# Kernel optimization log

Hardware: AMD Instinct MI355X
Metric: run time of the kernel (lower is better)

Reference implementation:

```python
import jax, jax.numpy as jnp
import numpy as np
from jax import lax

B, DIM, H, W = 4, 192, 128, 128
NUM_HEADS = 4
EPS = 1e-12


def _conv1x1(x, w):
    # x: [b,c,h,w], w: [o,i,1,1]
    return lax.conv_general_dilated(x, w, (1, 1), 'VALID',
                                    dimension_numbers=('NCHW', 'OIHW', 'NCHW'))


def _dwconv3x3(x, w):
    # depthwise: w: [c,1,3,3], groups = c
    return lax.conv_general_dilated(x, w, (1, 1), ((1, 1), (1, 1)),
                                    dimension_numbers=('NCHW', 'OIHW', 'NCHW'),
                                    feature_group_count=w.shape[0])


def _l2norm(t):
    # normalize along last (spatial) axis, torch F.normalize semantics
    n = jnp.sqrt(jnp.sum(t * t, axis=-1, keepdims=True))
    return t / jnp.maximum(n, EPS)


def _heads(t, b, h, w):
    # [b, head*c, h, w] -> [b, head, c, h*w]
    return t.reshape(b, NUM_HEADS, t.shape[1] // NUM_HEADS, h * w)


def setup_inputs() -> dict:
    key = jax.random.key(0)
    ks = jax.random.split(key, 9)
    s = 0.02
    return {
        'x': jax.random.normal(ks[0], (B, DIM, H, W), jnp.float32),
        'ctx': jax.random.normal(ks[1], (B, DIM, H, W), jnp.float32),
        'x_qkv_w': jax.random.normal(ks[2], (DIM * 3, DIM, 1, 1), jnp.float32) * s,
        'x_dw_w': jax.random.normal(ks[3], (DIM * 3, 1, 3, 3), jnp.float32) * s,
        'x_po_w': jax.random.normal(ks[4], (DIM, DIM, 1, 1), jnp.float32) * s,
        'ctx_qkv_w': jax.random.normal(ks[5], (DIM * 3, DIM, 1, 1), jnp.float32) * s,
        'ctx_dw_w': jax.random.normal(ks[6], (DIM * 3, 1, 3, 3), jnp.float32) * s,
        'ctx_po_w': jax.random.normal(ks[7], (DIM, DIM, 1, 1), jnp.float32) * s,
        'temperature': jnp.ones((NUM_HEADS, 1, 1), jnp.float32),
    }


def reference(x, ctx, x_qkv_w, x_dw_w, x_po_w, ctx_qkv_w, ctx_dw_w, ctx_po_w, temperature):
    b, c, h, w = x.shape
    x_qkv = _dwconv3x3(_conv1x1(x, x_qkv_w), x_dw_w)
    x_q, x_k, x_v = jnp.split(x_qkv, 3, axis=1)
    ctx_qkv = _dwconv3x3(_conv1x1(ctx, ctx_qkv_w), ctx_dw_w)
    ctx_q, ctx_k, ctx_v = jnp.split(ctx_qkv, 3, axis=1)

    x_q, x_k, x_v = (_heads(t, b, h, w) for t in (x_q, x_k, x_v))
    ctx_q, ctx_k, ctx_v = (_heads(t, b, h, w) for t in (ctx_q, ctx_k, ctx_v))

    temp = temperature[None]  # [1, head, 1, 1]

    # ctx branch: x_q attends over ctx
    q1 = _l2norm(x_q)
    k1 = _l2norm(ctx_k)
    attn1 = jax.nn.softmax(jnp.einsum('bhcn,bhdn->bhcd', q1, k1) * temp, axis=-1)
    ctx_out = jnp.einsum('bhcd,bhdn->bhcn', attn1, ctx_v).reshape(b, c, h, w)
    ctx_out = _conv1x1(ctx_out, ctx_po_w)

    # x branch: ctx_q attends over x
    q2 = _l2norm(ctx_q)
    k2 = _l2norm(x_k)
    attn2 = jax.nn.softmax(jnp.einsum('bhcn,bhdn->bhcd', q2, k2) * temp, axis=-1)
    x_out = jnp.einsum('bhcd,bhdn->bhcn', attn2, x_v).reshape(b, c, h, w)
    x_out = _conv1x1(x_out, x_po_w)

    return (x_out, ctx_out)
```

## Files before the change

### kernel.cpp

```cpp
#include <hip/hip_runtime.h>
#include <hip/hip_bf16.h>

#define N_PIX 16384
#define W_ 128

typedef __attribute__((ext_vector_type(8))) unsigned short ushort8_t;
typedef __attribute__((ext_vector_type(4))) unsigned short ushort4_t;
typedef __attribute__((ext_vector_type(8))) __bf16 bf16x8;
typedef __attribute__((ext_vector_type(4))) float f32x4;

__device__ inline float bf2f(unsigned short u) {
    return __uint_as_float(((unsigned)u) << 16);
}
__device__ inline unsigned short f2bf(float f) {
    __hip_bfloat16 h = __float2bfloat16(f);
    return *(unsigned short*)&h;
}

__global__ __launch_bounds__(256) void k_pack_w(
    const float* __restrict__ wa, const float* __restrict__ wb,
    unsigned short* __restrict__ oa, unsigned short* __restrict__ ob)
{
    const int blk = blockIdx.x;
    const float* w = (blk < 108) ? wa : wb;
    unsigned short* o = (blk < 108) ? oa : ob;
    const int i = ((blk % 108) * 256 + threadIdx.x) * 4;
    float4 v = *(const float4*)(w + i);
    ushort4_t s;
    s[0] = f2bf(v.x); s[1] = f2bf(v.y); s[2] = f2bf(v.z); s[3] = f2bf(v.w);
    *(ushort4_t*)(o + i) = s;
}

__global__ __launch_bounds__(512, 2) void k_conv_mfma(
    const float* __restrict__ x, const float* __restrict__ ctx,
    const unsigned short* __restrict__ wx, const unsigned short* __restrict__ wc,
    unsigned short* __restrict__ ox, unsigned short* __restrict__ octx)
{
    const int p0 = blockIdx.x * 128;
    const int bb = blockIdx.y;
    const int b  = bb & 3;
    const bool isx = bb < 4;
    const float* inb = (isx ? x : ctx) + (long)b * 192 * N_PIX;
    const unsigned short* wbf = isx ? wx : wc;
    unsigned short* ob = (isx ? ox : octx) + (long)b * 576 * N_PIX;

    __shared__ unsigned short Xl[128 * 200];

    const int tid  = threadIdx.x;
    const int lane = tid & 63;
    const int wid  = tid >> 6;
    const int wo   = wid >> 1;
    const int wp   = wid & 1;
    const int l15  = lane & 15;
    const int lq   = lane >> 4;

    {
        const int p = tid & 127, kh = tid >> 7;
        #pragma unroll
        for (int seg = 0; seg < 6; seg++) {
            ushort8_t pk;
            #pragma unroll
            for (int j = 0; j < 8; j++)
                pk[j] = f2bf(inb[(long)(kh * 48 + seg * 8 + j) * N_PIX + p0 + p]);
            *(ushort8_t*)&Xl[p * 200 + kh * 48 + seg * 8] = pk;
        }
    }
    __syncthreads();

    #pragma unroll 1
    for (int oc = 0; oc < 3; oc++) {
        const unsigned short* wrow = wbf + (long)(oc * 192 + wo * 48) * 192;

        bf16x8 afA[3], afB[3];
        #pragma unroll
        for (int mt = 0; mt < 3; mt++)
            afA[mt] = *(const bf16x8*)(wrow + (mt * 16 + l15) * 192 + lq * 8);

        f32x4 acc[3][4];
        const f32x4 zero = {0.f, 0.f, 0.f, 0.f};
        #pragma unroll
        for (int i = 0; i < 3; i++)
            #pragma unroll
            for (int j = 0; j < 4; j++) acc[i][j] = zero;

        #pragma unroll 1
        for (int kc2 = 0; kc2 < 3; kc2++) {
            const int kcA = kc2 * 2, kcB = kcA + 1;
            #pragma unroll
            for (int mt = 0; mt < 3; mt++)
                afB[mt] = *(const bf16x8*)(wrow + (mt * 16 + l15) * 192 + kcB * 32 + lq * 8);
            {
                bf16x8 bfv[4];
                #pragma unroll
                for (int nt = 0; nt < 4; nt++)
                    bfv[nt] = *(const bf16x8*)&Xl[(wp * 64 + nt * 16 + l15) * 200 + kcA * 32 + lq * 8];
                #pragma unroll
                for (int mt = 0; mt < 3; mt++)
                    #pragma unroll
                    for (int nt = 0; nt < 4; nt++)
                        acc[mt][nt] = __builtin_amdgcn_mfma_f32_16x16x32_bf16(
                            afA[mt], bfv[nt], acc[mt][nt], 0, 0, 0);
            }
            if (kc2 < 2) {
                #pragma unroll
                for (int mt = 0; mt < 3; mt++)
                    afA[mt] = *(const bf16x8*)(wrow + (mt * 16 + l15) * 192 + (kcA + 2) * 32 + lq * 8);
            }
            {
                bf16x8 bfv[4];
                #pragma unroll
                for (int nt = 0; nt < 4; nt++)
                    bfv[nt] = *(const bf16x8*)&Xl[(wp * 64 + nt * 16 + l15) * 200 + kcB * 32 + lq * 8];
                #pragma unroll
                for (int mt = 0; mt < 3; mt++)
                    #pragma unroll
                    for (int nt = 0; nt < 4; nt++)
                        acc[mt][nt] = __builtin_amdgcn_mfma_f32_16x16x32_bf16(
                            afB[mt], bfv[nt], acc[mt][nt], 0, 0, 0);
            }
        }

        #pragma unroll
        for (int mt = 0; mt < 3; mt++) {
            #pragma unroll
            for (int r = 0; r < 4; r++) {
                int o = oc * 192 + wo * 48 + mt * 16 + lq * 4 + r;
                long base = (long)o * N_PIX + p0 + wp * 64 + l15;
                #pragma unroll
                for (int nt = 0; nt < 4; nt++)
                    ob[base + nt * 16] = f2bf(acc[mt][nt][r]);
            }
        }
    }
}

__global__ __launch_bounds__(256) void k_dwconv(
    const unsigned short* __restrict__ tx, const unsigned short* __restrict__ tc,
    const float* __restrict__ wxd, const float* __restrict__ wcd,
    unsigned short* __restrict__ qx, unsigned short* __restrict__ qc)
{
    const int mz = blockIdx.y;
    const int br = (mz >= 2304) ? 1 : 0;
    const int m  = mz - br * 2304;
    const int ch = m % 576;
    const int y0 = blockIdx.x * 16;
    const unsigned short* ip = (br ? tc : tx) + (long)m * N_PIX;
    const float* wp = (br ? wcd : wxd) + ch * 9;
    unsigned short* op = (br ? qc : qx) + (long)m * N_PIX;

    __shared__ unsigned short Ll[18][136];

    const int tid = threadIdx.x;
    #pragma unroll
    for (int idx = tid; idx < 288; idx += 256) {
        int lr = idx >> 4, lc = (idx & 15) * 8;
        int gy = y0 - 1 + lr;
        ushort8_t v;
        #pragma unroll
        for (int j = 0; j < 8; j++) v[j] = 0;
        if ((unsigned)gy <= 127u)
            v = *(const ushort8_t*)(ip + gy * W_ + lc);
        *(ushort8_t*)&Ll[lr][lc] = v;
    }
    float wv[9];
    #pragma unroll
    for (int i = 0; i < 9; i++) wv[i] = wp[i];
    __syncthreads();

    const int r  = tid >> 4;
    const int xg = (tid & 15) * 8;

    float o[8];
    #pragma unroll
    for (int j = 0; j < 8; j++) o[j] = 0.f;

    #pragma unroll
    for (int dy = 0; dy < 3; dy++) {
        const unsigned short* lrow = &Ll[r + dy][0];
        float c[10];
        c[0] = (xg == 0) ? 0.f : bf2f(lrow[xg - 1]);
        ushort8_t mid = *(const ushort8_t*)&lrow[xg];
        #pragma unroll
        for (int j = 0; j < 8; j++) c[1 + j] = bf2f(mid[j]);
        c[9] = (xg == 120) ? 0.f : bf2f(lrow[xg + 8]);
        const float w0 = wv[dy * 3], w1 = wv[dy * 3 + 1], w2 = wv[dy * 3 + 2];
        #pragma unroll
        for (int j = 0; j < 8; j++)
            o[j] = fmaf(w0, c[j], fmaf(w1, c[j + 1], fmaf(w2, c[j + 2], o[j])));
    }
    ushort8_t res;
    #pragma unroll
    for (int j = 0; j < 8; j++) res[j] = f2bf(o[j]);
    *(ushort8_t*)(op + (y0 + r) * W_ + xg) = res;
}

__global__ __launch_bounds__(256) void k_gram_mfma(
    const unsigned short* __restrict__ qkv_x,
    const unsigned short* __restrict__ qkv_c,
    float* __restrict__ S, float* __restrict__ qn, float* __restrict__ kn)
{
    const int attn = blockIdx.z;
    const int bh   = blockIdx.y;
    const int b = bh >> 2, h = bh & 3;
    const unsigned short* qb =
        (attn == 0 ? qkv_x : qkv_c) + ((long)b * 576 + h * 48) * N_PIX;
    const unsigned short* kb =
        (attn == 0 ? qkv_c : qkv_x) + ((long)b * 576 + 192 + h * 48) * N_PIX;

    __shared__ float Sl[48 * 49];
    __shared__ float qnl[48], knl[48];

    const int tid = threadIdx.x;
    for (int i = tid; i < 48 * 49; i += 256) Sl[i] = 0.f;
    if (tid < 48) { qnl[tid] = 0.f; knl[tid] = 0.f; }
    __syncthreads();

    const int lane = tid & 63, wid = tid >> 6;
    const int l15 = lane & 15, lq = lane >> 4;
    const long nbase = (long)blockIdx.x * 1024 + wid * 256;

    f32x4 acc[3][3], aq[3], ak[3];
    const f32x4 zero = {0.f, 0.f, 0.f, 0.f};
    #pragma unroll
    for (int i = 0; i < 3; i++) {
        aq[i] = zero; ak[i] = zero;
        #pragma unroll
        for (int j = 0; j < 3; j++) acc[i][j] = zero;
    }

    for (int ks = 0; ks < 8; ks++) {
        const long ns = nbase + ks * 32;
        bf16x8 af[3], bfv[3];
        #pragma unroll
        for (int mt = 0; mt < 3; mt++)
            af[mt] = *(const bf16x8*)(qb + (long)(mt * 16 + l15) * N_PIX + ns + lq * 8);
        #pragma unroll
        for (int nt = 0; nt < 3; nt++)
            bfv[nt] = *(const bf16x8*)(kb + (long)(nt * 16 + l15) * N_PIX + ns + lq * 8);
        #pragma unroll
        for (int mt = 0; mt < 3; mt++)
            #pragma unroll
            for (int nt = 0; nt < 3; nt++)
                acc[mt][nt] = __builtin_amdgcn_mfma_f32_16x16x32_bf16(
                    af[mt], bfv[nt], acc[mt][nt], 0, 0, 0);
        #pragma unroll
        for (int mt = 0; mt < 3; mt++)
            aq[mt] = __builtin_amdgcn_mfma_f32_16x16x32_bf16(af[mt], af[mt], aq[mt], 0, 0, 0);
        #pragma unroll
        for (int nt = 0; nt < 3; nt++)
            ak[nt] = __builtin_amdgcn_mfma_f32_16x16x32_bf16(bfv[nt], bfv[nt], ak[nt], 0, 0, 0);
    }

    #pragma unroll
    for (int mt = 0; mt < 3; mt++)
        #pragma unroll
        for (int nt = 0; nt < 3; nt++)
            #pragma unroll
            for (int r = 0; r < 4; r++)
                atomicAdd(&Sl[(mt * 16 + lq * 4 + r) * 49 + nt * 16 + l15],
                          acc[mt][nt][r]);
    #pragma unroll
    for (int mt = 0; mt < 3; mt++)
        #pragma unroll
        for (int r = 0; r < 4; r++)
            if (l15 == lq * 4 + r) {
                atomicAdd(&qnl[mt * 16 + l15], aq[mt][r]);
                atomicAdd(&knl[mt * 16 + l15], ak[mt][r]);
            }
    __syncthreads();

    float* Sg = S + (long)(attn * 16 + bh) * 2304;
    float* qg = qn + (long)(attn * 16 + bh) * 48;
    float* kg = kn + (long)(attn * 16 + bh) * 48;
    for (int i = tid; i < 2304; i += 256) {
        int row = i / 48, col = i - row * 48;
        atomicAdd(&Sg[i], Sl[row * 49 + col]);
    }
    if (tid < 48) atomicAdd(&qg[tid], qnl[tid]);
    else if (tid < 96) atomicAdd(&kg[tid - 48], knl[tid - 48]);
}

__global__ __launch_bounds__(192) void k_softmax(
    const float* __restrict__ S, const float* __restrict__ qn,
    const float* __restrict__ kn, const float* __restrict__ temp,
    float* __restrict__ P)
{
    const int attn = blockIdx.x, b = blockIdx.y;
    const int r = threadIdx.x;
    const int h = r / 48, c = r % 48;
    const int bh = b * 4 + h;
    const float t = temp[h];
    const float* Srow = S + ((long)(attn * 16 + bh) * 48 + c) * 48;
    const float* knp  = kn + (long)(attn * 16 + bh) * 48;
    const float qc = fmaxf(sqrtf(qn[(long)(attn * 16 + bh) * 48 + c]), 1e-12f);
    float lg[48];
    float mx = -1e30f;
    #pragma unroll
    for (int d = 0; d < 48; d++) {
        float kd = fmaxf(sqrtf(knp[d]), 1e-12f);
        lg[d] = Srow[d] / (qc * kd) * t;
        mx = fmaxf(mx, lg[d]);
    }
    float sum = 0.f;
    #pragma unroll
    for (int d = 0; d < 48; d++) { lg[d] = __expf(lg[d] - mx); sum += lg[d]; }
    const float inv = 1.f / sum;
    float* Pp = P + (((long)(attn * 4 + b) * 4 + h) * 48 + c) * 48;
    #pragma unroll
    for (int d = 0; d < 48; d++) Pp[d] = lg[d] * inv;
}

__global__ __launch_bounds__(192) void k_w2(
    const float* __restrict__ P, const float* __restrict__ x_po,
    const float* __restrict__ ctx_po, unsigned short* __restrict__ W2)
{
    const int h = blockIdx.x, b = blockIdx.y, attn = blockIdx.z;
    const float* po = (attn == 0) ? ctx_po : x_po;
    __shared__ float Pl[48][48];
    const float* Pp = P + ((long)(attn * 4 + b) * 4 + h) * 2304;
    for (int it = 0; it < 12; it++) {
        int idx = it * 192 + threadIdx.x;
        Pl[idx / 48][idx % 48] = Pp[idx];
    }
    __syncthreads();
    const int o = threadIdx.x;
    float acc[48];
    #pragma unroll
    for (int d = 0; d < 48; d++) acc[d] = 0.f;
    for (int c = 0; c < 48; c++) {
        float pv = po[(long)o * 192 + h * 48 + c];
        #pragma unroll
        for (int d = 0; d < 48; d++)
            acc[d] = fmaf(pv, Pl[c][d], acc[d]);
    }
    unsigned short* wp = W2 + ((long)(attn * 4 + b) * 192 + o) * 192 + h * 48;
    #pragma unroll
    for (int d = 0; d < 48; d++) wp[d] = f2bf(acc[d]);
}

__global__ __launch_bounds__(512, 2) void k_gemm_v(
    const unsigned short* __restrict__ qkv_x,
    const unsigned short* __restrict__ qkv_c,
    const unsigned short* __restrict__ W2bf,
    float* __restrict__ out)
{
    const int p0 = blockIdx.x * 128;
    const int z  = blockIdx.y;
    const int br = z >> 2, b = z & 3;
    const unsigned short* v =
        (br == 0 ? qkv_x : qkv_c) + (long)b * 576 * N_PIX + 384L * N_PIX;
    const unsigned short* wb =
        W2bf + ((long)((br == 0 ? 1 : 0) * 4 + b)) * 36864;
    float* ob = out + (long)br * 12582912 + (long)b * 192 * N_PIX;

    __shared__ unsigned short Xl[128 * 200];

    const int tid  = threadIdx.x;
    const int lane = tid & 63;
    const int wid  = tid >> 6;
    const int wo   = wid >> 1;
    const int wp   = wid & 1;
    const int l15  = lane & 15;
    const int lq   = lane >> 4;

    {
        const int p = tid & 127, kh = tid >> 7;
        #pragma unroll
        for (int seg = 0; seg < 6; seg++) {
            ushort8_t pk;
            #pragma unroll
            for (int j = 0; j < 8; j++)
                pk[j] = v[(long)(kh * 48 + seg * 8 + j) * N_PIX + p0 + p];
            *(ushort8_t*)&Xl[p * 200 + kh * 48 + seg * 8] = pk;
        }
    }
    __syncthreads();

    const unsigned short* wrow = wb + (long)(wo * 48) * 192;

    bf16x8 afA[3], afB[3];
    #pragma unroll
    for (int mt = 0; mt < 3; mt++)
        afA[mt] = *(const bf16x8*)(wrow + (mt * 16 + l15) * 192 + lq * 8);

    f32x4 acc[3][4];
    const f32x4 zero = {0.f, 0.f, 0.f, 0.f};
    #pragma unroll
    for (int i = 0; i < 3; i++)
        #pragma unroll
        for (int j = 0; j < 4; j++) acc[i][j] = zero;

    #pragma unroll 1
    for (int kc2 = 0; kc2 < 3; kc2++) {
        const int kcA = kc2 * 2, kcB = kcA + 1;
        #pragma unroll
        for (int mt = 0; mt < 3; mt++)
            afB[mt] = *(const bf16x8*)(wrow + (mt * 16 + l15) * 192 + kcB * 32 + lq * 8);
        {
            bf16x8 bfv[4];
            #pragma unroll
            for (int nt = 0; nt < 4; nt++)
                bfv[nt] = *(const bf16x8*)&Xl[(wp * 64 + nt * 16 + l15) * 200 + kcA * 32 + lq * 8];
            #pragma unroll
            for (int mt = 0; mt < 3; mt++)
                #pragma unroll
                for (int nt = 0; nt < 4; nt++)
                    acc[mt][nt] = __builtin_amdgcn_mfma_f32_16x16x32_bf16(
                        afA[mt], bfv[nt], acc[mt][nt], 0, 0, 0);
        }
        if (kc2 < 2) {
            #pragma unroll
            for (int mt = 0; mt < 3; mt++)
                afA[mt] = *(const bf16x8*)(wrow + (mt * 16 + l15) * 192 + (kcA + 2) * 32 + lq * 8);
        }
        {
            bf16x8 bfv[4];
            #pragma unroll
            for (int nt = 0; nt < 4; nt++)
                bfv[nt] = *(const bf16x8*)&Xl[(wp * 64 + nt * 16 + l15) * 200 + kcB * 32 + lq * 8];
            #pragma unroll
            for (int mt = 0; mt < 3; mt++)
                #pragma unroll
                for (int nt = 0; nt < 4; nt++)
                    acc[mt][nt] = __builtin_amdgcn_mfma_f32_16x16x32_bf16(
                        afB[mt], bfv[nt], acc[mt][nt], 0, 0, 0);
        }
    }

    #pragma unroll
    for (int mt = 0; mt < 3; mt++) {
        #pragma unroll
        for (int r = 0; r < 4; r++) {
            int o = wo * 48 + mt * 16 + lq * 4 + r;
            long base = (long)o * N_PIX + p0 + wp * 64 + l15;
            #pragma unroll
            for (int nt = 0; nt < 4; nt++)
                ob[base + nt * 16] = acc[mt][nt][r];
        }
    }
}

extern "C" void kernel_launch(void* const* d_in, const int* in_sizes, int n_in,
                              void* d_out, int out_size, void* d_ws, size_t ws_size,
                              hipStream_t stream) {
    (void)in_sizes; (void)n_in; (void)out_size;
    const float* x       = (const float*)d_in[0];
    const float* ctx     = (const float*)d_in[1];
    const float* x_qkv_w = (const float*)d_in[2];
    const float* x_dw_w  = (const float*)d_in[3];
    const float* x_po_w  = (const float*)d_in[4];
    const float* c_qkv_w = (const float*)d_in[5];
    const float* c_dw_w  = (const float*)d_in[6];
    const float* c_po_w  = (const float*)d_in[7];
    const float* temp    = (const float*)d_in[8];
    float* out = (float*)d_out;

    const long QKV = 37748736L;
    unsigned short* qkv_x16 = (unsigned short*)d_ws;
    unsigned short* qkv_c16 = qkv_x16 + QKV;
    float* S  = (float*)(qkv_c16 + QKV);
    float* qn = S + 73728;
    float* kn = qn + 1536;
    float* P  = kn + 1536;
    unsigned short* W2bf = (unsigned short*)(P + 73728);

    unsigned short* tmp_x = (unsigned short*)d_out;
    unsigned short* wx16  = (unsigned short*)d_out + QKV;
    unsigned short* wc16  = wx16 + 110592;

    k_pack_w<<<dim3(216), 256, 0, stream>>>(x_qkv_w, c_qkv_w, wx16, wc16);

    const size_t ws_needed = (size_t)QKV * 2 * 3;
    if (ws_size >= ws_needed) {
        unsigned short* tmp_c = (unsigned short*)S;
        k_conv_mfma<<<dim3(128, 8), 512, 0, stream>>>(
            x, ctx, wx16, wc16, tmp_x, tmp_c);
        k_dwconv<<<dim3(8, 4608), 256, 0, stream>>>(
            tmp_x, tmp_c, x_dw_w, c_dw_w, qkv_x16, qkv_c16);
    } else {
        k_conv_mfma<<<dim3(128, 4), 512, 0, stream>>>(
            x, x, wx16, wx16, tmp_x, tmp_x);
        k_dwconv<<<dim3(8, 2304), 256, 0, stream>>>(
            tmp_x, tmp_x, x_dw_w, x_dw_w, qkv_x16, qkv_x16);
        k_conv_mfma<<<dim3(128, 4), 512, 0, stream>>>(
            ctx, ctx, wc16, wc16, tmp_x, tmp_x);
        k_dwconv<<<dim3(8, 2304), 256, 0, stream>>>(
            tmp_x, tmp_x, c_dw_w, c_dw_w, qkv_c16, qkv_c16);
    }

    hipMemsetAsync(S, 0, (73728 + 1536 + 1536) * sizeof(float), stream);

    k_gram_mfma<<<dim3(16, 16, 2), 256, 0, stream>>>(qkv_x16, qkv_c16, S, qn, kn);
    k_softmax<<<dim3(2, 4), dim3(192), 0, stream>>>(S, qn, kn, temp, P);
    k_w2<<<dim3(4, 4, 2), dim3(192), 0, stream>>>(P, x_po_w, c_po_w, W2bf);

    k_gemm_v<<<dim3(128, 8), 512, 0, stream>>>(qkv_x16, qkv_c16, W2bf, out);
}
```

Measured before the change: 412.2 us.

## Halve pixel tiles in conv and V-GEMM kernels; fuse softmax with W2 build

The 1x1-conv and final V-GEMM kernels now run 256-thread blocks over 64-pixel tiles instead of 512-thread blocks over 128 pixels. This doubles the grid size and allows more resident blocks per CU, while the MFMA inner loop loads one B fragment at a time to lower register pressure. The softmax and P·W_po kernels are merged into one kernel that keeps P in shared memory, which removes a launch and the global round trip for P. The trade-off is that each fused block runs four heads serially on only 8 blocks, and each weight fragment is reused across fewer pixels.

```diff
diff --git a/kernel.cpp b/kernel.cpp
--- a/kernel.cpp
+++ b/kernel.cpp
@@ -31,12 +31,12 @@
     *(ushort4_t*)(o + i) = s;
 }
 
-__global__ __launch_bounds__(512, 2) void k_conv_mfma(
+__global__ __launch_bounds__(256, 4) void k_conv_mfma(
     const float* __restrict__ x, const float* __restrict__ ctx,
     const unsigned short* __restrict__ wx, const unsigned short* __restrict__ wc,
     unsigned short* __restrict__ ox, unsigned short* __restrict__ octx)
 {
-    const int p0 = blockIdx.x * 128;
+    const int p0 = blockIdx.x * 64;
     const int bb = blockIdx.y;
     const int b  = bb & 3;
     const bool isx = bb < 4;
@@ -44,18 +44,16 @@
     const unsigned short* wbf = isx ? wx : wc;
     unsigned short* ob = (isx ? ox : octx) + (long)b * 576 * N_PIX;
 
-    __shared__ unsigned short Xl[128 * 200];
+    __shared__ unsigned short Xl[64 * 200];
 
     const int tid  = threadIdx.x;
     const int lane = tid & 63;
-    const int wid  = tid >> 6;
-    const int wo   = wid >> 1;
-    const int wp   = wid & 1;
+    const int wo   = tid >> 6;
     const int l15  = lane & 15;
     const int lq   = lane >> 4;
 
     {
-        const int p = tid & 127, kh = tid >> 7;
+        const int p = tid & 63, kh = tid >> 6;
         #pragma unroll
         for (int seg = 0; seg < 6; seg++) {
             ushort8_t pk;
@@ -89,34 +87,26 @@
             #pragma unroll
             for (int mt = 0; mt < 3; mt++)
                 afB[mt] = *(const bf16x8*)(wrow + (mt * 16 + l15) * 192 + kcB * 32 + lq * 8);
-            {
-                bf16x8 bfv[4];
-                #pragma unroll
-                for (int nt = 0; nt < 4; nt++)
-                    bfv[nt] = *(const bf16x8*)&Xl[(wp * 64 + nt * 16 + l15) * 200 + kcA * 32 + lq * 8];
+            #pragma unroll
+            for (int nt = 0; nt < 4; nt++) {
+                bf16x8 bfv = *(const bf16x8*)&Xl[(nt * 16 + l15) * 200 + kcA * 32 + lq * 8];
                 #pragma unroll
                 for (int mt = 0; mt < 3; mt++)
-                    #pragma unroll
-                    for (int nt = 0; nt < 4; nt++)
-                        acc[mt][nt] = __builtin_amdgcn_mfma_f32_16x16x32_bf16(
-                            afA[mt], bfv[nt], acc[mt][nt], 0, 0, 0);
+                    acc[mt][nt] = __builtin_amdgcn_mfma_f32_16x16x32_bf16(
+                        afA[mt], bfv, acc[mt][nt], 0, 0, 0);
             }
             if (kc2 < 2) {
                 #pragma unroll
                 for (int mt = 0; mt < 3; mt++)
                     afA[mt] = *(const bf16x8*)(wrow + (mt * 16 + l15) * 192 + (kcA + 2) * 32 + lq * 8);
             }
-            {
-                bf16x8 bfv[4];
-                #pragma unroll
-                for (int nt = 0; nt < 4; nt++)
-                    bfv[nt] = *(const bf16x8*)&Xl[(wp * 64 + nt * 16 + l15) * 200 + kcB * 32 + lq * 8];
+            #pragma unroll
+            for (int nt = 0; nt < 4; nt++) {
+                bf16x8 bfv = *(const bf16x8*)&Xl[(nt * 16 + l15) * 200 + kcB * 32 + lq * 8];
                 #pragma unroll
                 for (int mt = 0; mt < 3; mt++)
-                    #pragma unroll
-                    for (int nt = 0; nt < 4; nt++)
-                        acc[mt][nt] = __builtin_amdgcn_mfma_f32_16x16x32_bf16(
-                            afB[mt], bfv[nt], acc[mt][nt], 0, 0, 0);
+                    acc[mt][nt] = __builtin_amdgcn_mfma_f32_16x16x32_bf16(
+                        afB[mt], bfv, acc[mt][nt], 0, 0, 0);
             }
         }
 
@@ -125,7 +115,7 @@
             #pragma unroll
             for (int r = 0; r < 4; r++) {
                 int o = oc * 192 + wo * 48 + mt * 16 + lq * 4 + r;
-                long base = (long)o * N_PIX + p0 + wp * 64 + l15;
+                long base = (long)o * N_PIX + p0 + l15;
                 #pragma unroll
                 for (int nt = 0; nt < 4; nt++)
                     ob[base + nt * 16] = f2bf(acc[mt][nt][r]);
@@ -280,71 +270,68 @@
     else if (tid < 96) atomicAdd(&kg[tid - 48], knl[tid - 48]);
 }
 
-__global__ __launch_bounds__(192) void k_softmax(
+__global__ __launch_bounds__(192) void k_sm_w2(
     const float* __restrict__ S, const float* __restrict__ qn,
     const float* __restrict__ kn, const float* __restrict__ temp,
-    float* __restrict__ P)
+    const float* __restrict__ x_po, const float* __restrict__ ctx_po,
+    unsigned short* __restrict__ W2)
 {
     const int attn = blockIdx.x, b = blockIdx.y;
-    const int r = threadIdx.x;
-    const int h = r / 48, c = r % 48;
-    const int bh = b * 4 + h;
-    const float t = temp[h];
-    const float* Srow = S + ((long)(attn * 16 + bh) * 48 + c) * 48;
-    const float* knp  = kn + (long)(attn * 16 + bh) * 48;
-    const float qc = fmaxf(sqrtf(qn[(long)(attn * 16 + bh) * 48 + c]), 1e-12f);
-    float lg[48];
-    float mx = -1e30f;
-    #pragma unroll
-    for (int d = 0; d < 48; d++) {
-        float kd = fmaxf(sqrtf(knp[d]), 1e-12f);
-        lg[d] = Srow[d] / (qc * kd) * t;
-        mx = fmaxf(mx, lg[d]);
-    }
-    float sum = 0.f;
-    #pragma unroll
-    for (int d = 0; d < 48; d++) { lg[d] = __expf(lg[d] - mx); sum += lg[d]; }
-    const float inv = 1.f / sum;
-    float* Pp = P + (((long)(attn * 4 + b) * 4 + h) * 48 + c) * 48;
-    #pragma unroll
-    for (int d = 0; d < 48; d++) Pp[d] = lg[d] * inv;
-}
-
-__global__ __launch_bounds__(192) void k_w2(
-    const float* __restrict__ P, const float* __restrict__ x_po,
-    const float* __restrict__ ctx_po, unsigned short* __restrict__ W2)
-{
-    const int h = blockIdx.x, b = blockIdx.y, attn = blockIdx.z;
-    const float* po = (attn == 0) ? ctx_po : x_po;
-    __shared__ float Pl[48][48];
-    const float* Pp = P + ((long)(attn * 4 + b) * 4 + h) * 2304;
-    for (int it = 0; it < 12; it++) {
-        int idx = it * 192 + threadIdx.x;
-        Pl[idx / 48][idx % 48] = Pp[idx];
-    }
-    __syncthreads();
-    const int o = threadIdx.x;
-    float acc[48];
-    #pragma unroll
-    for (int d = 0; d < 48; d++) acc[d] = 0.f;
-    for (int c = 0; c < 48; c++) {
-        float pv = po[(long)o * 192 + h * 48 + c];
-        #pragma unroll
-        for (int d = 0; d < 48; d++)
-            acc[d] = fmaf(pv, Pl[c][d], acc[d]);
-    }
-    unsigned short* wp = W2 + ((long)(attn * 4 + b) * 192 + o) * 192 + h * 48;
-    #pragma unroll
-    for (int d = 0; d < 48; d++) wp[d] = f2bf(acc[d]);
-}
-
-__global__ __launch_bounds__(512, 2) void k_gemm_v(
+    __shared__ float Pl[4][48][48];
+
+    {
+        const int r = threadIdx.x;
+        const int h = r / 48, c = r % 48;
+        const int bh = b * 4 + h;
+        const float t = temp[h];
+        const float* Srow = S + ((long)(attn * 16 + bh) * 48 + c) * 48;
+        const float* knp  = kn + (long)(attn * 16 + bh) * 48;
+        const float qc = fmaxf(sqrtf(qn[(long)(attn * 16 + bh) * 48 + c]), 1e-12f);
+        float lg[48];
+        float mx = -1e30f;
+        #pragma unroll
+        for (int d = 0; d < 48; d++) {
+            float kd = fmaxf(sqrtf(knp[d]), 1e-12f);
+            lg[d] = Srow[d] / (qc * kd) * t;
+            mx = fmaxf(mx, lg[d]);
+        }
+        float sum = 0.f;
+        #pragma unroll
+        for (int d = 0; d < 48; d++) { lg[d] = __expf(lg[d] - mx); sum += lg[d]; }
+        const float inv = 1.f / sum;
+        #pragma unroll
+        for (int d = 0; d < 48; d++) Pl[h][c][d] = lg[d] * inv;
+    }
+    __syncthreads();
+
+    {
+        const float* po = (attn == 0) ? ctx_po : x_po;
+        const int o = threadIdx.x;
+        unsigned short* wp = W2 + ((long)(attn * 4 + b) * 192 + o) * 192;
+        #pragma unroll 1
+        for (int h = 0; h < 4; h++) {
+            float acc[48];
+            #pragma unroll
+            for (int d = 0; d < 48; d++) acc[d] = 0.f;
+            for (int c = 0; c < 48; c++) {
+                float pv = po[(long)o * 192 + h * 48 + c];
+                #pragma unroll
+                for (int d = 0; d < 48; d++)
+                    acc[d] = fmaf(pv, Pl[h][c][d], acc[d]);
+            }
+            #pragma unroll
+            for (int d = 0; d < 48; d++) wp[h * 48 + d] = f2bf(acc[d]);
+        }
+    }
+}
+
+__global__ __launch_bounds__(256, 4) void k_gemm_v(
     const unsigned short* __restrict__ qkv_x,
     const unsigned short* __restrict__ qkv_c,
     const unsigned short* __restrict__ W2bf,
     float* __restrict__ out)
 {
-    const int p0 = blockIdx.x * 128;
+    const int p0 = blockIdx.x * 64;
     const int z  = blockIdx.y;
     const int br = z >> 2, b = z & 3;
     const unsigned short* v =
@@ -353,18 +340,16 @@
         W2bf + ((long)((br == 0 ? 1 : 0) * 4 + b)) * 36864;
     float* ob = out + (long)br * 12582912 + (long)b * 192 * N_PIX;
 
-    __shared__ unsigned short Xl[128 * 200];
+    __shared__ unsigned short Xl[64 * 200];
 
     const int tid  = threadIdx.x;
     const int lane = tid & 63;
-    const int wid  = tid >> 6;
-    const int wo   = wid >> 1;
-    const int wp   = wid & 1;
+    const int wo   = tid >> 6;
     const int l15  = lane & 15;
     const int lq   = lane >> 4;
 
     {
-        const int p = tid & 127, kh = tid >> 7;
+        const int p = tid & 63, kh = tid >> 6;
         #pragma unroll
         for (int seg = 0; seg < 6; seg++) {
             ushort8_t pk;
@@ -396,34 +381,26 @@
         #pragma unroll
         for (int mt = 0; mt < 3; mt++)
             afB[mt] = *(const bf16x8*)(wrow + (mt * 16 + l15) * 192 + kcB * 32 + lq * 8);
-        {
-            bf16x8 bfv[4];
-            #pragma unroll
-            for (int nt = 0; nt < 4; nt++)
-                bfv[nt] = *(const bf16x8*)&Xl[(wp * 64 + nt * 16 + l15) * 200 + kcA * 32 + lq * 8];
+        #pragma unroll
+        for (int nt = 0; nt < 4; nt++) {
+            bf16x8 bfv = *(const bf16x8*)&Xl[(nt * 16 + l15) * 200 + kcA * 32 + lq * 8];
             #pragma unroll
             for (int mt = 0; mt < 3; mt++)
-                #pragma unroll
-                for (int nt = 0; nt < 4; nt++)
-                    acc[mt][nt] = __builtin_amdgcn_mfma_f32_16x16x32_bf16(
-                        afA[mt], bfv[nt], acc[mt][nt], 0, 0, 0);
+                acc[mt][nt] = __builtin_amdgcn_mfma_f32_16x16x32_bf16(
+                    afA[mt], bfv, acc[mt][nt], 0, 0, 0);
         }
         if (kc2 < 2) {
             #pragma unroll
             for (int mt = 0; mt < 3; mt++)
                 afA[mt] = *(const bf16x8*)(wrow + (mt * 16 + l15) * 192 + (kcA + 2) * 32 + lq * 8);
         }
-        {
-            bf16x8 bfv[4];
-            #pragma unroll
-            for (int nt = 0; nt < 4; nt++)
-                bfv[nt] = *(const bf16x8*)&Xl[(wp * 64 + nt * 16 + l15) * 200 + kcB * 32 + lq * 8];
+        #pragma unroll
+        for (int nt = 0; nt < 4; nt++) {
+            bf16x8 bfv = *(const bf16x8*)&Xl[(nt * 16 + l15) * 200 + kcB * 32 + lq * 8];
             #pragma unroll
             for (int mt = 0; mt < 3; mt++)
-                #pragma unroll
-                for (int nt = 0; nt < 4; nt++)
-                    acc[mt][nt] = __builtin_amdgcn_mfma_f32_16x16x32_bf16(
-                        afB[mt], bfv[nt], acc[mt][nt], 0, 0, 0);
+                acc[mt][nt] = __builtin_amdgcn_mfma_f32_16x16x32_bf16(
+                    afB[mt], bfv, acc[mt][nt], 0, 0, 0);
         }
     }
 
@@ -432,7 +409,7 @@
         #pragma unroll
         for (int r = 0; r < 4; r++) {
             int o = wo * 48 + mt * 16 + lq * 4 + r;
-            long base = (long)o * N_PIX + p0 + wp * 64 + l15;
+            long base = (long)o * N_PIX + p0 + l15;
             #pragma unroll
             for (int nt = 0; nt < 4; nt++)
                 ob[base + nt * 16] = acc[mt][nt][r];
@@ -461,8 +438,7 @@
     float* S  = (float*)(qkv_c16 + QKV);
     float* qn = S + 73728;
     float* kn = qn + 1536;
-    float* P  = kn + 1536;
-    unsigned short* W2bf = (unsigned short*)(P + 73728);
+    unsigned short* W2bf = (unsigned short*)(kn + 1536);
 
     unsigned short* tmp_x = (unsigned short*)d_out;
     unsigned short* wx16  = (unsigned short*)d_out + QKV;
@@ -473,16 +449,16 @@
     const size_t ws_needed = (size_t)QKV * 2 * 3;
     if (ws_size >= ws_needed) {
         unsigned short* tmp_c = (unsigned short*)S;
-        k_conv_mfma<<<dim3(128, 8), 512, 0, stream>>>(
+        k_conv_mfma<<<dim3(256, 8), 256, 0, stream>>>(
             x, ctx, wx16, wc16, tmp_x, tmp_c);
         k_dwconv<<<dim3(8, 4608), 256, 0, stream>>>(
             tmp_x, tmp_c, x_dw_w, c_dw_w, qkv_x16, qkv_c16);
     } else {
-        k_conv_mfma<<<dim3(128, 4), 512, 0, stream>>>(
+        k_conv_mfma<<<dim3(256, 4), 256, 0, stream>>>(
             x, x, wx16, wx16, tmp_x, tmp_x);
         k_dwconv<<<dim3(8, 2304), 256, 0, stream>>>(
             tmp_x, tmp_x, x_dw_w, x_dw_w, qkv_x16, qkv_x16);
-        k_conv_mfma<<<dim3(128, 4), 512, 0, stream>>>(
+        k_conv_mfma<<<dim3(256, 4), 256, 0, stream>>>(
             ctx, ctx, wc16, wc16, tmp_x, tmp_x);
         k_dwconv<<<dim3(8, 2304), 256, 0, stream>>>(
             tmp_x, tmp_x, c_dw_w, c_dw_w, qkv_c16, qkv_c16);
@@ -491,8 +467,8 @@
     hipMemsetAsync(S, 0, (73728 + 1536 + 1536) * sizeof(float), stream);
 
     k_gram_mfma<<<dim3(16, 16, 2), 256, 0, stream>>>(qkv_x16, qkv_c16, S, qn, kn);
-    k_softmax<<<dim3(2, 4), dim3(192), 0, stream>>>(S, qn, kn, temp, P);
-    k_w2<<<dim3(4, 4, 2), dim3(192), 0, stream>>>(P, x_po_w, c_po_w, W2bf);
-
-    k_gemm_v<<<dim3(128, 8), 512, 0, stream>>>(qkv_x16, qkv_c16, W2bf, out);
-}
+    k_sm_w2<<<dim3(2, 4), dim3(192), 0, stream>>>(
+        S, qn, kn, temp, x_po_w, c_po_w, W2bf);
+
+    k_gemm_v<<<dim3(256, 8), 256, 0, stream>>>(qkv_x16, qkv_c16, W2bf, out);
+}
```

New measurement: 483.6 us. 1.17x slower.
